# Performance work log

Hardware: AMD Instinct MI355X
Metric: run time of the kernel (lower is better)

Reference implementation:

```python
import jax, jax.numpy as jnp
import numpy as np

B, L, N_IN, N_STATE = 32, 4096, 8, 8
C_IN, C_OUT = N_IN + N_STATE, N_STATE
H, M, N_LAYERS = 64, 64, 4


def setup_inputs() -> dict:
    key = jax.random.key(0)
    ks = jax.random.split(key, 16)
    s = 0.02
    return {
        "u": jax.random.normal(ks[0], (B, L, N_IN), jnp.float32),
        "z": jax.random.normal(ks[1], (B, N_STATE), jnp.float32),
        "t": jax.random.uniform(ks[2], (B, 1), jnp.float32),
        "w_lift": jax.random.normal(ks[3], (H, C_IN), jnp.float32) * s,
        "b_lift": jnp.zeros((H,), jnp.float32),
        "spec_wr": jax.random.normal(ks[4], (N_LAYERS, H, H, M), jnp.float32) / (H),
        "spec_wi": jax.random.normal(ks[5], (N_LAYERS, H, H, M), jnp.float32) / (H),
        "w_skip": jax.random.normal(ks[6], (N_LAYERS, H, H), jnp.float32) * s,
        "b_skip": jnp.zeros((N_LAYERS, H), jnp.float32),
        "w_p1": jax.random.normal(ks[7], (2 * H, H), jnp.float32) * s,
        "b_p1": jnp.zeros((2 * H,), jnp.float32),
        "w_p2": jax.random.normal(ks[8], (C_OUT, 2 * H), jnp.float32) * s,
        "b_p2": jnp.zeros((C_OUT,), jnp.float32),
    }


def _fno_forward(u, z, w_lift, b_lift, spec_wr, spec_wi, w_skip, b_skip, w_p1, b_p1, w_p2, b_p2):
    b, l, _ = u.shape
    rep_z = jnp.broadcast_to(z[:, None, :], (b, l, z.shape[1]))
    x = jnp.concatenate([u, rep_z], axis=-1)          # [B, L, C_in]
    x = jnp.transpose(x, (0, 2, 1))                   # [B, C_in, L]
    # lifting (1x1 conv)
    x = jnp.einsum("bcl,hc->bhl", x, w_lift) + b_lift[None, :, None]
    n_layers, _, _, m = spec_wr.shape
    for i in range(n_layers):
        xf = jnp.fft.rfft(x, axis=-1)                 # [B, H, L//2+1] complex
        w = spec_wr[i] + 1j * spec_wi[i]              # [H, H, M]
        of = jnp.einsum("bim,oim->bom", xf[..., :m], w)
        of = jnp.pad(of, ((0, 0), (0, 0), (0, xf.shape[-1] - m)))
        xs = jnp.fft.irfft(of, n=l, axis=-1)          # [B, H, L]
        sk = jnp.einsum("bil,oi->bol", x, w_skip[i]) + b_skip[i][None, :, None]
        x = xs + sk
        if i < n_layers - 1:
            x = jax.nn.gelu(x)
    # projection: H -> 2H -> C_out (1x1 convs)
    x = jax.nn.gelu(jnp.einsum("bhl,ph->bpl", x, w_p1) + b_p1[None, :, None])
    x = jnp.einsum("bpl,op->bol", x, w_p2) + b_p2[None, :, None]
    outs = jnp.transpose(x, (0, 2, 1))                # [B, L, C_out]
    return outs[:, -1, :]                             # [B, C_out]


def reference(u, z, t, w_lift, b_lift, spec_wr, spec_wi, w_skip, b_skip, w_p1, b_p1, w_p2, b_p2):
    # t is accepted by the original forward but unused in FNOProjection
    return _fno_forward(u, z, w_lift, b_lift, spec_wr, spec_wi, w_skip, b_skip, w_p1, b_p1, w_p2, b_p2)
```

## Files before the change

### kernel.cpp

```cpp
#include <hip/hip_runtime.h>
#include <math.h>

typedef _Float16 f16;
typedef f16  f16x2 __attribute__((ext_vector_type(2)));
typedef f16  f16x4 __attribute__((ext_vector_type(4)));
typedef f16  f16x8 __attribute__((ext_vector_type(8)));
typedef float f32x4 __attribute__((ext_vector_type(4)));

#define F4(p)  (*(float4*)(p))
#define CF4(p) (*(const float4*)(p))

namespace {
constexpr int LL = 4096;
constexpr int HH = 64;

__device__ __forceinline__ float gelu_fast(float x) {
    float inner = 0.7978845608028654f * (x + 0.044715f * x * x * x);
    float e = __expf(-2.0f * inner);
    return x / (1.0f + e);
}

__device__ __forceinline__ f32x4 mfma16(f16x8 a, f16x8 b, f32x4 c) {
    return __builtin_amdgcn_mfma_f32_16x16x32_f16(a, b, c, 0, 0, 0);
}
}

__global__ __launch_bounds__(256) void k_init(const float* __restrict__ u,
                                              const float* __restrict__ z,
                                              const float* __restrict__ wl,
                                              const float* __restrict__ bl,
                                              const float* __restrict__ wsk,
                                              const float* __restrict__ wr,
                                              const float* __restrict__ wi,
                                              f16* __restrict__ Tdt,
                                              f16* __restrict__ Ttr,
                                              f16* __restrict__ wskh,
                                              f16* __restrict__ wrh,
                                              f16* __restrict__ wih,
                                              f16* __restrict__ XT0) {
    const int bid = blockIdx.x;
    const int t = threadIdx.x;
    if (bid < 512) {
        const int b = bid >> 4;
        const int l0 = (bid & 15) * 256;
        constexpr int IP = 260;
        __shared__ float in_s[16 * IP];
        __shared__ float wsh[64 * 16];
        __shared__ float bsh[64];
        for (int i = t; i < 1024; i += 256) wsh[i] = wl[i];
        if (t < 64) bsh[t] = bl[t];
#pragma unroll
        for (int q = 0; q < 2; ++q) {
            int f = t + q * 256;
            int l = f >> 1, cq = (f & 1) * 4;
            float4 v = CF4(u + ((size_t)b * LL + l0 + l) * 8 + cq);
            in_s[(cq + 0) * IP + l] = v.x;
            in_s[(cq + 1) * IP + l] = v.y;
            in_s[(cq + 2) * IP + l] = v.z;
            in_s[(cq + 3) * IP + l] = v.w;
        }
        for (int f = t; f < 8 * 256; f += 256) {
            int c = f >> 8, l = f & 255;
            in_s[(8 + c) * IP + l] = z[b * 8 + c];
        }
        __syncthreads();
        const int hg = t >> 5, lsub = t & 31;
        float acc[8][8] = {};
        for (int c = 0; c < 16; ++c) {
            float wv[8], inv[8];
#pragma unroll
            for (int i = 0; i < 8; ++i) wv[i] = wsh[(hg * 8 + i) * 16 + c];
#pragma unroll
            for (int j = 0; j < 8; ++j) inv[j] = in_s[c * IP + lsub + 32 * j];
#pragma unroll
            for (int i = 0; i < 8; ++i)
#pragma unroll
                for (int j = 0; j < 8; ++j) acc[i][j] += wv[i] * inv[j];
        }
#pragma unroll
        for (int j = 0; j < 8; ++j) {
            __attribute__((aligned(16))) f16 hv[8];
#pragma unroll
            for (int i = 0; i < 8; ++i) hv[i] = (f16)(acc[i][j] + bsh[hg * 8 + i]);
            int l = l0 + lsub + 32 * j;
            F4(XT0 + ((size_t)b * LL + l) * HH + hg * 8) = CF4(hv);
        }
    } else if (bid < 1536) {
        const int tb = bid - 512;
        const float w0 = 6.283185307179586f / 4096.0f;
        {
            int m = tb >> 4;
            int l = ((tb & 15) << 8) + t;
            float s, c;
            sincosf((float)((l * m) & 4095) * w0, &s, &c);
            Tdt[(size_t)(2 * m) * LL + l]     = (f16)c;
            Tdt[(size_t)(2 * m + 1) * LL + l] = (f16)(-s);
        }
        {
            int l = tb * 4 + (t >> 6);
            int m = t & 63;
            float s, c;
            sincosf((float)((l * m) & 4095) * w0, &s, &c);
            const float sc = 1.0f / 4096.0f;
            f16x2 pv;
            pv.x = (f16)((m == 0) ? sc : 2.0f * sc * c);
            pv.y = (f16)((m == 0) ? 0.0f : -2.0f * sc * s);
            *(f16x2*)(Ttr + (size_t)l * 128 + 2 * m) = pv;
        }
        if (tb < 64) {
            int idx = tb * 256 + t;
            wskh[idx] = (f16)wsk[idx];
        }
    } else {
        const int cb = bid - 1536;
        size_t base = (size_t)cb * 1024 + t * 4;
        float4 vr = CF4(wr + base);
        float4 vi = CF4(wi + base);
        f16x4 hr, hi;
        hr.x = (f16)vr.x; hr.y = (f16)vr.y; hr.z = (f16)vr.z; hr.w = (f16)vr.w;
        hi.x = (f16)vi.x; hi.y = (f16)vi.y; hi.z = (f16)vi.z; hi.w = (f16)vi.w;
        *(f16x4*)(wrh + base) = hr;
        *(f16x4*)(wih + base) = hi;
    }
}

__global__ __launch_bounds__(256) void k_dft(const f16* __restrict__ XT,
                                             const f16* __restrict__ Tdt,
                                             f16* __restrict__ Y) {
    __shared__ f16 Asl[32 * 72];
    __shared__ f16 Bsl[128 * 72];
    const int t = threadIdx.x;
    const int ch = blockIdx.x >> 1, h0 = (blockIdx.x & 1) * 32, b = blockIdx.y;
    const int lane = t & 63, wid = t >> 6;
    const int mh = (wid & 1) * 16, n0 = (wid >> 1) * 64;
    const int fm = lane & 15, fq = lane >> 4;
    f32x4 acc[4] = {};
    for (int k0 = 0; k0 < 512; k0 += 64) {
        const int l0 = ch * 512 + k0;
        __syncthreads();
        {
            int seg = t >> 6;
            f16x8 v = *(const f16x8*)(XT + ((size_t)b * LL + l0 + lane) * HH + h0 + seg * 8);
#pragma unroll
            for (int i = 0; i < 8; ++i) Asl[(seg * 8 + i) * 72 + lane] = v[i];
        }
#pragma unroll
        for (int p = 0; p < 4; ++p) {
            int r = (t >> 3) + p * 32;
            F4(&Bsl[r * 72 + (t & 7) * 8]) = CF4(Tdt + (size_t)r * LL + l0 + (t & 7) * 8);
        }
        __syncthreads();
#pragma unroll
        for (int ks = 0; ks < 64; ks += 32) {
            f16x8 a = *(const f16x8*)&Asl[(mh + fm) * 72 + ks + fq * 8];
#pragma unroll
            for (int j = 0; j < 4; ++j) {
                f16x8 bj = *(const f16x8*)&Bsl[(n0 + j * 16 + fm) * 72 + ks + fq * 8];
                acc[j] = mfma16(a, bj, acc[j]);
            }
        }
    }
    f16* yp = Y + ((size_t)ch * 2048 + b * HH + h0) * 128;
#pragma unroll
    for (int j = 0; j < 4; ++j)
#pragma unroll
        for (int r = 0; r < 4; ++r)
            yp[(size_t)(mh + fq * 4 + r) * 128 + n0 + j * 16 + fm] = (f16)acc[j][r];
}

__global__ __launch_bounds__(256) void k_spec(const f16* __restrict__ Y,
                                              const f16* __restrict__ wrh,
                                              const f16* __restrict__ wih,
                                              f16* __restrict__ Ofh, int layer) {
    __shared__ float xsh[64 * 128];
    const int t = threadIdx.x;
    const int b = blockIdx.x;
    const int og = blockIdx.y;
    {
#pragma unroll
        for (int i = 0; i < 4; ++i) {
            int g = t + i * 256;
            float s[8] = {};
#pragma unroll
            for (int c = 0; c < 8; ++c) {
                f16x8 v = *(const f16x8*)(Y + ((size_t)c * 2048 + b * HH) * 128 + g * 8);
#pragma unroll
                for (int e = 0; e < 8; ++e) s[e] += (float)v[e];
            }
#pragma unroll
            for (int e = 0; e < 8; ++e) xsh[g * 8 + e] = s[e];
        }
    }
    __syncthreads();
    const int m = t & 63, osub = t >> 6;
    const int o = og * 4 + osub;
    const f16* wrp = wrh + ((size_t)layer * HH + o) * HH * 64 + m;
    const f16* wip = wih + ((size_t)layer * HH + o) * HH * 64 + m;
    float are = 0.0f, aim = 0.0f;
    const float2* xs2 = (const float2*)xsh;
#pragma unroll 8
    for (int i = 0; i < 64; ++i) {
        float2 xv = xs2[i * 64 + m];
        float wrv = (float)wrp[(size_t)i * 64];
        float wiv = (float)wip[(size_t)i * 64];
        are += xv.x * wrv - xv.y * wiv;
        aim += xv.x * wiv + xv.y * wrv;
    }
    f16x2 ov; ov.x = (f16)are; ov.y = (f16)aim;
    *(f16x2*)(Ofh + ((size_t)b * HH + o) * 128 + 2 * m) = ov;
}

__global__ __launch_bounds__(256) void k_recon(const f16* __restrict__ Ofh,
                                               const f16* __restrict__ XT,
                                               const f16* __restrict__ Ttr,
                                               const f16* __restrict__ wskh,
                                               const float* __restrict__ bsk,
                                               f16* __restrict__ XTn,
                                               int layer) {
    __shared__ f16 Asl[64 * 200];
    __shared__ f16 Bsl[128 * 72];
    const int t = threadIdx.x;
    const int l0 = blockIdx.x * 128, b = blockIdx.y;
    const int lane = t & 63, wid = t >> 6;
    const int m0 = (wid & 1) * 32, n0 = (wid >> 1) * 64;
    const int fm = lane & 15, fq = lane >> 4;
    f32x4 acc[2][4] = {};
    {
        int seg = t & 15, row = t >> 4;
#pragma unroll
        for (int p = 0; p < 4; ++p) {
            int r = row + p * 16;
            F4(&Asl[r * 200 + seg * 8]) = CF4(Ofh + ((size_t)(b * HH + r)) * 128 + seg * 8);
        }
        int seg8 = t & 7, row8 = t >> 3;
#pragma unroll
        for (int p = 0; p < 2; ++p) {
            int r = row8 + p * 32;
            F4(&Asl[r * 200 + 128 + seg8 * 8]) =
                CF4(wskh + ((size_t)(layer * HH + r)) * HH + seg8 * 8);
        }
    }
    const int srow = t >> 3, sseg = t & 7;
    for (int k0 = 0; k0 < 192; k0 += 64) {
        __syncthreads();
#pragma unroll
        for (int p = 0; p < 4; ++p) {
            int r = srow + p * 32;
            const f16* src = (k0 < 128)
                ? (Ttr + (size_t)(l0 + r) * 128 + k0 + sseg * 8)
                : (XT + ((size_t)b * LL + l0 + r) * HH + sseg * 8);
            F4(&Bsl[r * 72 + sseg * 8]) = CF4(src);
        }
        __syncthreads();
#pragma unroll
        for (int ks = 0; ks < 64; ks += 32) {
            f16x8 a0 = *(const f16x8*)&Asl[(m0 + fm) * 200 + k0 + ks + fq * 8];
            f16x8 a1 = *(const f16x8*)&Asl[(m0 + 16 + fm) * 200 + k0 + ks + fq * 8];
#pragma unroll
            for (int j = 0; j < 4; ++j) {
                f16x8 bj = *(const f16x8*)&Bsl[(n0 + j * 16 + fm) * 72 + ks + fq * 8];
                acc[0][j] = mfma16(a0, bj, acc[0][j]);
                acc[1][j] = mfma16(a1, bj, acc[1][j]);
            }
        }
    }
    __syncthreads();
#pragma unroll
    for (int i = 0; i < 2; ++i)
#pragma unroll
        for (int r = 0; r < 4; ++r) {
            int row = m0 + i * 16 + fq * 4 + r;
            float bias = bsk[layer * HH + row];
#pragma unroll
            for (int j = 0; j < 4; ++j) {
                float v = gelu_fast(acc[i][j][r] + bias);
                int lc = n0 + j * 16 + fm;
                Bsl[lc * 72 + row] = (f16)v;
            }
        }
    __syncthreads();
    {
        int row = t >> 1, half = t & 1;
        f16* dst = XTn + ((size_t)b * LL + l0 + row) * HH + half * 32;
        const f16* src = &Bsl[row * 72 + half * 32];
#pragma unroll
        for (int i = 0; i < 4; ++i)
            F4(dst + i * 8) = CF4(src + i * 8);
    }
}

__global__ __launch_bounds__(128) void k_final(const f16* __restrict__ Ofh,
                                               const f16* __restrict__ XT3,
                                               const f16* __restrict__ Ttr,
                                               const float* __restrict__ wsk,
                                               const float* __restrict__ bsk,
                                               const float* __restrict__ wp1,
                                               const float* __restrict__ bp1,
                                               const float* __restrict__ wp2,
                                               const float* __restrict__ bp2,
                                               float* __restrict__ out) {
    __shared__ float ofs[64 * 129];
    __shared__ float wsks[64 * 65];
    __shared__ float wp1s[128 * 65];
    __shared__ float tl[128], xl[64], x4[64], y[128];
    const int b = blockIdx.x, t = threadIdx.x;
    {
#pragma unroll
        for (int i = 0; i < 8; ++i) {
            int g = t + i * 128;
            f16x8 v = *(const f16x8*)(Ofh + (size_t)b * HH * 128 + g * 8);
            int o = g >> 4, k0 = (g & 15) * 8;
#pragma unroll
            for (int e = 0; e < 8; ++e) ofs[o * 129 + k0 + e] = (float)v[e];
        }
    }
    {
        const float* src = wsk + 3 * HH * HH;
#pragma unroll
        for (int i = 0; i < 8; ++i) {
            int g = t + i * 128;
            float4 v = CF4(src + g * 4);
            int o = g >> 4, c0 = (g & 15) * 4;
            F4(&wsks[o * 65 + c0]) = v;
        }
    }
    {
#pragma unroll
        for (int i = 0; i < 16; ++i) {
            int g = t + i * 128;
            float4 v = CF4(wp1 + g * 4);
            int p = g >> 4, c0 = (g & 15) * 4;
            F4(&wp1s[p * 65 + c0]) = v;
        }
    }
    tl[t] = (float)Ttr[(size_t)(LL - 1) * 128 + t];
    if (t < 64) xl[t] = (float)XT3[((size_t)b * LL + (LL - 1)) * HH + t];
    __syncthreads();
    if (t < 64) {
        const int o = t;
        float acc = bsk[3 * HH + o];
        for (int k = 0; k < 128; ++k) acc += ofs[o * 129 + k] * tl[k];
        for (int i = 0; i < 64; ++i) acc += wsks[o * 65 + i] * xl[i];
        x4[o] = acc;
    }
    __syncthreads();
    {
        float acc = bp1[t];
        for (int h = 0; h < 64; ++h) acc += wp1s[t * 65 + h] * x4[h];
        y[t] = gelu_fast(acc);
    }
    __syncthreads();
    if (t < 8) {
        float acc = bp2[t];
        for (int p = 0; p < 128; ++p) acc += wp2[t * 128 + p] * y[p];
        out[b * 8 + t] = acc;
    }
}

extern "C" void kernel_launch(void* const* d_in, const int* in_sizes, int n_in,
                              void* d_out, int out_size, void* d_ws, size_t ws_size,
                              hipStream_t stream) {
    (void)in_sizes; (void)n_in; (void)out_size; (void)ws_size;
    const float* u   = (const float*)d_in[0];
    const float* z   = (const float*)d_in[1];
    const float* wl  = (const float*)d_in[3];
    const float* bl  = (const float*)d_in[4];
    const float* swr = (const float*)d_in[5];
    const float* swi = (const float*)d_in[6];
    const float* wsk = (const float*)d_in[7];
    const float* bsk = (const float*)d_in[8];
    const float* wp1 = (const float*)d_in[9];
    const float* bp1 = (const float*)d_in[10];
    const float* wp2 = (const float*)d_in[11];
    const float* bp2 = (const float*)d_in[12];
    float* out = (float*)d_out;

    f16* ws    = (f16*)d_ws;
    f16* XTa   = ws;
    f16* XTb   = XTa + 8388608;
    f16* Tdt   = XTb + 8388608;
    f16* Ttr   = Tdt + 524288;
    f16* Ofh   = Ttr + 524288;
    f16* wskh  = Ofh + 262144;
    f16* wrh   = wskh + 16384;
    f16* wih   = wrh + 1048576;

    k_init<<<2560, 256, 0, stream>>>(u, z, wl, bl, wsk, swr, swi,
                                     Tdt, Ttr, wskh, wrh, wih, XTa);

    f16* xtc = XTa; f16* xtn = XTb;
    for (int layer = 0; layer < 4; ++layer) {
        f16* Y = xtn;
        k_dft<<<dim3(16, 32), 256, 0, stream>>>(xtc, Tdt, Y);
        k_spec<<<dim3(32, 16), 256, 0, stream>>>(Y, wrh, wih, Ofh, layer);
        if (layer < 3) {
            k_recon<<<dim3(32, 32), 256, 0, stream>>>(Ofh, xtc, Ttr, wskh, bsk,
                                                      xtn, layer);
            f16* tmp = xtc; xtc = xtn; xtn = tmp;
        } else {
            k_final<<<32, 128, 0, stream>>>(Ofh, xtc, Ttr, wsk, bsk,
                                            wp1, bp1, wp2, bp2, out);
        }
    }
}
```

Measured before the change: 213.4 us.

## Fuse truncated forward DFT into lifting and reconstruction kernels

New measurement: 248.5 us. 16.5% more time.

```diff
diff --git a/kernel.cpp b/kernel.cpp
--- a/kernel.cpp
+++ b/kernel.cpp
@@ -25,68 +25,18 @@
 }
 }
 
-__global__ __launch_bounds__(256) void k_init(const float* __restrict__ u,
-                                              const float* __restrict__ z,
-                                              const float* __restrict__ wl,
-                                              const float* __restrict__ bl,
-                                              const float* __restrict__ wsk,
-                                              const float* __restrict__ wr,
-                                              const float* __restrict__ wi,
-                                              f16* __restrict__ Tdt,
-                                              f16* __restrict__ Ttr,
-                                              f16* __restrict__ wskh,
-                                              f16* __restrict__ wrh,
-                                              f16* __restrict__ wih,
-                                              f16* __restrict__ XT0) {
+__global__ __launch_bounds__(256) void k_tw(const float* __restrict__ wsk,
+                                            const float* __restrict__ wr,
+                                            const float* __restrict__ wi,
+                                            f16* __restrict__ Tdt,
+                                            f16* __restrict__ Ttr,
+                                            f16* __restrict__ wskh,
+                                            f16* __restrict__ wrh,
+                                            f16* __restrict__ wih) {
     const int bid = blockIdx.x;
     const int t = threadIdx.x;
-    if (bid < 512) {
-        const int b = bid >> 4;
-        const int l0 = (bid & 15) * 256;
-        constexpr int IP = 260;
-        __shared__ float in_s[16 * IP];
-        __shared__ float wsh[64 * 16];
-        __shared__ float bsh[64];
-        for (int i = t; i < 1024; i += 256) wsh[i] = wl[i];
-        if (t < 64) bsh[t] = bl[t];
-#pragma unroll
-        for (int q = 0; q < 2; ++q) {
-            int f = t + q * 256;
-            int l = f >> 1, cq = (f & 1) * 4;
-            float4 v = CF4(u + ((size_t)b * LL + l0 + l) * 8 + cq);
-            in_s[(cq + 0) * IP + l] = v.x;
-            in_s[(cq + 1) * IP + l] = v.y;
-            in_s[(cq + 2) * IP + l] = v.z;
-            in_s[(cq + 3) * IP + l] = v.w;
-        }
-        for (int f = t; f < 8 * 256; f += 256) {
-            int c = f >> 8, l = f & 255;
-            in_s[(8 + c) * IP + l] = z[b * 8 + c];
-        }
-        __syncthreads();
-        const int hg = t >> 5, lsub = t & 31;
-        float acc[8][8] = {};
-        for (int c = 0; c < 16; ++c) {
-            float wv[8], inv[8];
-#pragma unroll
-            for (int i = 0; i < 8; ++i) wv[i] = wsh[(hg * 8 + i) * 16 + c];
-#pragma unroll
-            for (int j = 0; j < 8; ++j) inv[j] = in_s[c * IP + lsub + 32 * j];
-#pragma unroll
-            for (int i = 0; i < 8; ++i)
-#pragma unroll
-                for (int j = 0; j < 8; ++j) acc[i][j] += wv[i] * inv[j];
-        }
-#pragma unroll
-        for (int j = 0; j < 8; ++j) {
-            __attribute__((aligned(16))) f16 hv[8];
-#pragma unroll
-            for (int i = 0; i < 8; ++i) hv[i] = (f16)(acc[i][j] + bsh[hg * 8 + i]);
-            int l = l0 + lsub + 32 * j;
-            F4(XT0 + ((size_t)b * LL + l) * HH + hg * 8) = CF4(hv);
-        }
-    } else if (bid < 1536) {
-        const int tb = bid - 512;
+    if (bid < 1024) {
+        const int tb = bid;
         const float w0 = 6.283185307179586f / 4096.0f;
         {
             int m = tb >> 4;
@@ -112,7 +62,7 @@
             wskh[idx] = (f16)wsk[idx];
         }
     } else {
-        const int cb = bid - 1536;
+        const int cb = bid - 1024;
         size_t base = (size_t)cb * 1024 + t * 4;
         float4 vr = CF4(wr + base);
         float4 vi = CF4(wi + base);
@@ -124,48 +74,102 @@
     }
 }
 
-__global__ __launch_bounds__(256) void k_dft(const f16* __restrict__ XT,
-                                             const f16* __restrict__ Tdt,
-                                             f16* __restrict__ Y) {
-    __shared__ f16 Asl[32 * 72];
-    __shared__ f16 Bsl[128 * 72];
+__global__ __launch_bounds__(256) void k_lift(const float* __restrict__ u,
+                                              const float* __restrict__ z,
+                                              const float* __restrict__ wl,
+                                              const float* __restrict__ bl,
+                                              const f16* __restrict__ Tdt,
+                                              f16* __restrict__ XT0,
+                                              f16* __restrict__ Y) {
+    __shared__ __attribute__((aligned(16))) f16 pool[26112];
+    __shared__ float bsh[64];
+    float* in_s = (float*)pool;
+    float* wsh  = (float*)pool + 4160;
+    f16* Xh  = pool;
+    f16* Bsl = pool + 16896;
+    constexpr int IP = 260;
     const int t = threadIdx.x;
-    const int ch = blockIdx.x >> 1, h0 = (blockIdx.x & 1) * 32, b = blockIdx.y;
+    const int lt = blockIdx.x, b = blockIdx.y;
+    const int l0 = lt * 256;
+    for (int i = t; i < 1024; i += 256) wsh[i] = wl[i];
+    if (t < 64) bsh[t] = bl[t];
+#pragma unroll
+    for (int q = 0; q < 2; ++q) {
+        int f = t + q * 256;
+        int l = f >> 1, cq = (f & 1) * 4;
+        float4 v = CF4(u + ((size_t)b * LL + l0 + l) * 8 + cq);
+        in_s[(cq + 0) * IP + l] = v.x;
+        in_s[(cq + 1) * IP + l] = v.y;
+        in_s[(cq + 2) * IP + l] = v.z;
+        in_s[(cq + 3) * IP + l] = v.w;
+    }
+    for (int f = t; f < 8 * 256; f += 256) {
+        int c = f >> 8, l = f & 255;
+        in_s[(8 + c) * IP + l] = z[b * 8 + c];
+    }
+    __syncthreads();
+    const int hg = t >> 5, lsub = t & 31;
+    float acc[8][8] = {};
+    for (int c = 0; c < 16; ++c) {
+        float wv[8], inv[8];
+#pragma unroll
+        for (int i = 0; i < 8; ++i) wv[i] = wsh[(hg * 8 + i) * 16 + c];
+#pragma unroll
+        for (int j = 0; j < 8; ++j) inv[j] = in_s[c * IP + lsub + 32 * j];
+#pragma unroll
+        for (int i = 0; i < 8; ++i)
+#pragma unroll
+            for (int j = 0; j < 8; ++j) acc[i][j] += wv[i] * inv[j];
+    }
+    __syncthreads();
+#pragma unroll
+    for (int j = 0; j < 8; ++j) {
+        __attribute__((aligned(16))) f16 hv[8];
+#pragma unroll
+        for (int i = 0; i < 8; ++i) hv[i] = (f16)(acc[i][j] + bsh[hg * 8 + i]);
+        int l = l0 + lsub + 32 * j;
+        F4(XT0 + ((size_t)b * LL + l) * HH + hg * 8) = CF4(hv);
+#pragma unroll
+        for (int i = 0; i < 8; ++i)
+            Xh[(hg * 8 + i) * 264 + lsub + 32 * j] = hv[i];
+    }
     const int lane = t & 63, wid = t >> 6;
-    const int mh = (wid & 1) * 16, n0 = (wid >> 1) * 64;
     const int fm = lane & 15, fq = lane >> 4;
-    f32x4 acc[4] = {};
-    for (int k0 = 0; k0 < 512; k0 += 64) {
-        const int l0 = ch * 512 + k0;
-        __syncthreads();
-        {
-            int seg = t >> 6;
-            f16x8 v = *(const f16x8*)(XT + ((size_t)b * LL + l0 + lane) * HH + h0 + seg * 8);
-#pragma unroll
-            for (int i = 0; i < 8; ++i) Asl[(seg * 8 + i) * 72 + lane] = v[i];
-        }
-#pragma unroll
-        for (int p = 0; p < 4; ++p) {
-            int r = (t >> 3) + p * 32;
-            F4(&Bsl[r * 72 + (t & 7) * 8]) = CF4(Tdt + (size_t)r * LL + l0 + (t & 7) * 8);
-        }
-        __syncthreads();
-#pragma unroll
-        for (int ks = 0; ks < 64; ks += 32) {
-            f16x8 a = *(const f16x8*)&Asl[(mh + fm) * 72 + ks + fq * 8];
-#pragma unroll
-            for (int j = 0; j < 4; ++j) {
-                f16x8 bj = *(const f16x8*)&Bsl[(n0 + j * 16 + fm) * 72 + ks + fq * 8];
-                acc[j] = mfma16(a, bj, acc[j]);
-            }
-        }
-    }
-    f16* yp = Y + ((size_t)ch * 2048 + b * HH + h0) * 128;
-#pragma unroll
-    for (int j = 0; j < 4; ++j)
-#pragma unroll
-        for (int r = 0; r < 4; ++r)
-            yp[(size_t)(mh + fq * 4 + r) * 128 + n0 + j * 16 + fm] = (f16)acc[j][r];
+    const int n0d = wid * 32;
+    for (int half = 0; half < 2; ++half) {
+        f32x4 acc2[4][2] = {};
+        for (int kc = 0; kc < 2; ++kc) {
+            __syncthreads();
+#pragma unroll
+            for (int p = 0; p < 4; ++p) {
+                int r = (t >> 3) + p * 32;
+                F4(&Bsl[r * 72 + (t & 7) * 8]) =
+                    CF4(Tdt + (size_t)r * LL + l0 + half * 128 + kc * 64 + (t & 7) * 8);
+            }
+            __syncthreads();
+#pragma unroll
+            for (int ks = 0; ks < 64; ks += 32) {
+                f16x8 a[4];
+#pragma unroll
+                for (int i = 0; i < 4; ++i)
+                    a[i] = *(const f16x8*)&Xh[(fm + 16 * i) * 264 + half * 128 + kc * 64 + ks + fq * 8];
+#pragma unroll
+                for (int j = 0; j < 2; ++j) {
+                    f16x8 bj = *(const f16x8*)&Bsl[(n0d + j * 16 + fm) * 72 + ks + fq * 8];
+#pragma unroll
+                    for (int i = 0; i < 4; ++i) acc2[i][j] = mfma16(a[i], bj, acc2[i][j]);
+                }
+            }
+        }
+        f16* yp = Y + ((size_t)(lt * 2 + half) * 2048 + b * 64) * 128;
+#pragma unroll
+        for (int i = 0; i < 4; ++i)
+#pragma unroll
+            for (int j = 0; j < 2; ++j)
+#pragma unroll
+                for (int r = 0; r < 4; ++r)
+                    yp[(size_t)(i * 16 + fq * 4 + r) * 128 + n0d + j * 16 + fm] = (f16)acc2[i][j][r];
+    }
 }
 
 __global__ __launch_bounds__(256) void k_spec(const f16* __restrict__ Y,
@@ -181,8 +185,7 @@
         for (int i = 0; i < 4; ++i) {
             int g = t + i * 256;
             float s[8] = {};
-#pragma unroll
-            for (int c = 0; c < 8; ++c) {
+            for (int c = 0; c < 32; ++c) {
                 f16x8 v = *(const f16x8*)(Y + ((size_t)c * 2048 + b * HH) * 128 + g * 8);
 #pragma unroll
                 for (int e = 0; e < 8; ++e) s[e] += (float)v[e];
@@ -213,14 +216,20 @@
 __global__ __launch_bounds__(256) void k_recon(const f16* __restrict__ Ofh,
                                                const f16* __restrict__ XT,
                                                const f16* __restrict__ Ttr,
+                                               const f16* __restrict__ Tdt,
                                                const f16* __restrict__ wskh,
                                                const float* __restrict__ bsk,
                                                f16* __restrict__ XTn,
+                                               f16* __restrict__ Y,
                                                int layer) {
-    __shared__ f16 Asl[64 * 200];
-    __shared__ f16 Bsl[128 * 72];
+    __shared__ __attribute__((aligned(16))) f16 pool[27136];
+    f16* Amain = pool;
+    f16* Bmain = pool + 12800;
+    f16* Ash   = pool;
+    f16* Xsl   = pool + 8704;
+    f16* B2    = pool + 17920;
     const int t = threadIdx.x;
-    const int l0 = blockIdx.x * 128, b = blockIdx.y;
+    const int lt = blockIdx.x, l0 = lt * 128, b = blockIdx.y;
     const int lane = t & 63, wid = t >> 6;
     const int m0 = (wid & 1) * 32, n0 = (wid >> 1) * 64;
     const int fm = lane & 15, fq = lane >> 4;
@@ -230,13 +239,13 @@
 #pragma unroll
         for (int p = 0; p < 4; ++p) {
             int r = row + p * 16;
-            F4(&Asl[r * 200 + seg * 8]) = CF4(Ofh + ((size_t)(b * HH + r)) * 128 + seg * 8);
+            F4(&Amain[r * 200 + seg * 8]) = CF4(Ofh + ((size_t)(b * HH + r)) * 128 + seg * 8);
         }
         int seg8 = t & 7, row8 = t >> 3;
 #pragma unroll
         for (int p = 0; p < 2; ++p) {
             int r = row8 + p * 32;
-            F4(&Asl[r * 200 + 128 + seg8 * 8]) =
+            F4(&Amain[r * 200 + 128 + seg8 * 8]) =
                 CF4(wskh + ((size_t)(layer * HH + r)) * HH + seg8 * 8);
         }
     }
@@ -249,16 +258,16 @@
             const f16* src = (k0 < 128)
                 ? (Ttr + (size_t)(l0 + r) * 128 + k0 + sseg * 8)
                 : (XT + ((size_t)b * LL + l0 + r) * HH + sseg * 8);
-            F4(&Bsl[r * 72 + sseg * 8]) = CF4(src);
+            F4(&Bmain[r * 72 + sseg * 8]) = CF4(src);
         }
         __syncthreads();
 #pragma unroll
         for (int ks = 0; ks < 64; ks += 32) {
-            f16x8 a0 = *(const f16x8*)&Asl[(m0 + fm) * 200 + k0 + ks + fq * 8];
-            f16x8 a1 = *(const f16x8*)&Asl[(m0 + 16 + fm) * 200 + k0 + ks + fq * 8];
+            f16x8 a0 = *(const f16x8*)&Amain[(m0 + fm) * 200 + k0 + ks + fq * 8];
+            f16x8 a1 = *(const f16x8*)&Amain[(m0 + 16 + fm) * 200 + k0 + ks + fq * 8];
 #pragma unroll
             for (int j = 0; j < 4; ++j) {
-                f16x8 bj = *(const f16x8*)&Bsl[(n0 + j * 16 + fm) * 72 + ks + fq * 8];
+                f16x8 bj = *(const f16x8*)&Bmain[(n0 + j * 16 + fm) * 72 + ks + fq * 8];
                 acc[0][j] = mfma16(a0, bj, acc[0][j]);
                 acc[1][j] = mfma16(a1, bj, acc[1][j]);
             }
@@ -274,19 +283,54 @@
 #pragma unroll
             for (int j = 0; j < 4; ++j) {
                 float v = gelu_fast(acc[i][j][r] + bias);
+                f16 hv = (f16)v;
                 int lc = n0 + j * 16 + fm;
-                Bsl[lc * 72 + row] = (f16)v;
+                Xsl[lc * 72 + row] = hv;
+                Ash[row * 136 + lc] = hv;
             }
         }
     __syncthreads();
     {
         int row = t >> 1, half = t & 1;
         f16* dst = XTn + ((size_t)b * LL + l0 + row) * HH + half * 32;
-        const f16* src = &Bsl[row * 72 + half * 32];
+        const f16* src = &Xsl[row * 72 + half * 32];
 #pragma unroll
         for (int i = 0; i < 4; ++i)
             F4(dst + i * 8) = CF4(src + i * 8);
     }
+    const int n0d = wid * 32;
+    f32x4 acc2[4][2] = {};
+    for (int kc = 0; kc < 2; ++kc) {
+        __syncthreads();
+#pragma unroll
+        for (int p = 0; p < 4; ++p) {
+            int r = (t >> 3) + p * 32;
+            F4(&B2[r * 72 + (t & 7) * 8]) =
+                CF4(Tdt + (size_t)r * LL + l0 + kc * 64 + (t & 7) * 8);
+        }
+        __syncthreads();
+#pragma unroll
+        for (int ks = 0; ks < 64; ks += 32) {
+            f16x8 a[4];
+#pragma unroll
+            for (int i = 0; i < 4; ++i)
+                a[i] = *(const f16x8*)&Ash[(fm + 16 * i) * 136 + kc * 64 + ks + fq * 8];
+#pragma unroll
+            for (int j = 0; j < 2; ++j) {
+                f16x8 bj = *(const f16x8*)&B2[(n0d + j * 16 + fm) * 72 + ks + fq * 8];
+#pragma unroll
+                for (int i = 0; i < 4; ++i) acc2[i][j] = mfma16(a[i], bj, acc2[i][j]);
+            }
+        }
+    }
+    f16* yp = Y + ((size_t)lt * 2048 + b * 64) * 128;
+#pragma unroll
+    for (int i = 0; i < 4; ++i)
+#pragma unroll
+        for (int j = 0; j < 2; ++j)
+#pragma unroll
+            for (int r = 0; r < 4; ++r)
+                yp[(size_t)(i * 16 + fq * 4 + r) * 128 + n0d + j * 16 + fm] = (f16)acc2[i][j][r];
 }
 
 __global__ __launch_bounds__(128) void k_final(const f16* __restrict__ Ofh,
@@ -378,24 +422,23 @@
     f16* ws    = (f16*)d_ws;
     f16* XTa   = ws;
     f16* XTb   = XTa + 8388608;
-    f16* Tdt   = XTb + 8388608;
+    f16* Yb    = XTb + 8388608;
+    f16* Tdt   = Yb + 8388608;
     f16* Ttr   = Tdt + 524288;
     f16* Ofh   = Ttr + 524288;
     f16* wskh  = Ofh + 262144;
     f16* wrh   = wskh + 16384;
     f16* wih   = wrh + 1048576;
 
-    k_init<<<2560, 256, 0, stream>>>(u, z, wl, bl, wsk, swr, swi,
-                                     Tdt, Ttr, wskh, wrh, wih, XTa);
+    k_tw<<<2048, 256, 0, stream>>>(wsk, swr, swi, Tdt, Ttr, wskh, wrh, wih);
+    k_lift<<<dim3(16, 32), 256, 0, stream>>>(u, z, wl, bl, Tdt, XTa, Yb);
 
     f16* xtc = XTa; f16* xtn = XTb;
     for (int layer = 0; layer < 4; ++layer) {
-        f16* Y = xtn;
-        k_dft<<<dim3(16, 32), 256, 0, stream>>>(xtc, Tdt, Y);
-        k_spec<<<dim3(32, 16), 256, 0, stream>>>(Y, wrh, wih, Ofh, layer);
+        k_spec<<<dim3(32, 16), 256, 0, stream>>>(Yb, wrh, wih, Ofh, layer);
         if (layer < 3) {
-            k_recon<<<dim3(32, 32), 256, 0, stream>>>(Ofh, xtc, Ttr, wskh, bsk,
-                                                      xtn, layer);
+            k_recon<<<dim3(32, 32), 256, 0, stream>>>(Ofh, xtc, Ttr, Tdt, wskh,
+                                                      bsk, xtn, Yb, layer);
             f16* tmp = xtc; xtc = xtn; xtn = tmp;
         } else {
             k_final<<<32, 128, 0, stream>>>(Ofh, xtc, Ttr, wsk, bsk,
```

## Fuse DFT and spectral mixing into a single kernel without split-L partials

Applied to the files above, without the earlier changes.

After: 317.0 us. 48.6% more time.

```diff
diff --git a/kernel.cpp b/kernel.cpp
--- a/kernel.cpp
+++ b/kernel.cpp
@@ -124,90 +124,69 @@
     }
 }
 
-__global__ __launch_bounds__(256) void k_dft(const f16* __restrict__ XT,
-                                             const f16* __restrict__ Tdt,
-                                             f16* __restrict__ Y) {
-    __shared__ f16 Asl[32 * 72];
-    __shared__ f16 Bsl[128 * 72];
+__global__ __launch_bounds__(1024) void k_dftspec(const f16* __restrict__ XT,
+                                                  const f16* __restrict__ Tdt,
+                                                  const f16* __restrict__ wrh,
+                                                  const f16* __restrict__ wih,
+                                                  f16* __restrict__ Ofh, int layer) {
+    __shared__ __attribute__((aligned(16))) f16 pool[17408];
+    f16* Asl = pool;
+    f16* Bsl = pool + 8704;
+    float* xsh = (float*)pool;
+    const int bid = blockIdx.x;
+    const int b = bid & 31, mhalf = bid >> 5;
     const int t = threadIdx.x;
-    const int ch = blockIdx.x >> 1, h0 = (blockIdx.x & 1) * 32, b = blockIdx.y;
-    const int lane = t & 63, wid = t >> 6;
-    const int mh = (wid & 1) * 16, n0 = (wid >> 1) * 64;
+    const int wid = t >> 6, lane = t & 63;
+    const int wm = wid & 3, wn = wid >> 2;
     const int fm = lane & 15, fq = lane >> 4;
-    f32x4 acc[4] = {};
-    for (int k0 = 0; k0 < 512; k0 += 64) {
-        const int l0 = ch * 512 + k0;
-        __syncthreads();
-        {
-            int seg = t >> 6;
-            f16x8 v = *(const f16x8*)(XT + ((size_t)b * LL + l0 + lane) * HH + h0 + seg * 8);
-#pragma unroll
-            for (int i = 0; i < 8; ++i) Asl[(seg * 8 + i) * 72 + lane] = v[i];
-        }
-#pragma unroll
-        for (int p = 0; p < 4; ++p) {
-            int r = (t >> 3) + p * 32;
-            F4(&Bsl[r * 72 + (t & 7) * 8]) = CF4(Tdt + (size_t)r * LL + l0 + (t & 7) * 8);
-        }
-        __syncthreads();
-#pragma unroll
-        for (int ks = 0; ks < 64; ks += 32) {
-            f16x8 a = *(const f16x8*)&Asl[(mh + fm) * 72 + ks + fq * 8];
-#pragma unroll
-            for (int j = 0; j < 4; ++j) {
-                f16x8 bj = *(const f16x8*)&Bsl[(n0 + j * 16 + fm) * 72 + ks + fq * 8];
-                acc[j] = mfma16(a, bj, acc[j]);
-            }
-        }
-    }
-    f16* yp = Y + ((size_t)ch * 2048 + b * HH + h0) * 128;
-#pragma unroll
-    for (int j = 0; j < 4; ++j)
-#pragma unroll
-        for (int r = 0; r < 4; ++r)
-            yp[(size_t)(mh + fq * 4 + r) * 128 + n0 + j * 16 + fm] = (f16)acc[j][r];
-}
-
-__global__ __launch_bounds__(256) void k_spec(const f16* __restrict__ Y,
-                                              const f16* __restrict__ wrh,
-                                              const f16* __restrict__ wih,
-                                              f16* __restrict__ Ofh, int layer) {
-    __shared__ float xsh[64 * 128];
-    const int t = threadIdx.x;
-    const int b = blockIdx.x;
-    const int og = blockIdx.y;
-    {
-#pragma unroll
-        for (int i = 0; i < 4; ++i) {
-            int g = t + i * 256;
-            float s[8] = {};
-#pragma unroll
-            for (int c = 0; c < 8; ++c) {
-                f16x8 v = *(const f16x8*)(Y + ((size_t)c * 2048 + b * HH) * 128 + g * 8);
-#pragma unroll
-                for (int e = 0; e < 8; ++e) s[e] += (float)v[e];
-            }
-#pragma unroll
-            for (int e = 0; e < 8; ++e) xsh[g * 8 + e] = s[e];
-        }
-    }
-    __syncthreads();
-    const int m = t & 63, osub = t >> 6;
-    const int o = og * 4 + osub;
-    const f16* wrp = wrh + ((size_t)layer * HH + o) * HH * 64 + m;
-    const f16* wip = wih + ((size_t)layer * HH + o) * HH * 64 + m;
-    float are = 0.0f, aim = 0.0f;
-    const float2* xs2 = (const float2*)xsh;
+    const int sa_seg = t >> 7, sa_l = t & 127;
+    const int sb_row = t >> 4, sb_seg = t & 15;
+
+    f16x8 ra = *(const f16x8*)(XT + ((size_t)b * LL + sa_l) * HH + sa_seg * 8);
+    f16x8 rb = *(const f16x8*)(Tdt + (size_t)(mhalf * 64 + sb_row) * LL + sb_seg * 8);
+    f32x4 acc = {};
+    for (int c = 0; c < 32; ++c) {
+        __syncthreads();
+#pragma unroll
+        for (int i = 0; i < 8; ++i) Asl[(sa_seg * 8 + i) * 136 + sa_l] = ra[i];
+        *(f16x8*)&Bsl[sb_row * 136 + sb_seg * 8] = rb;
+        __syncthreads();
+        if (c < 31) {
+            int l0 = (c + 1) * 128;
+            ra = *(const f16x8*)(XT + ((size_t)b * LL + l0 + sa_l) * HH + sa_seg * 8);
+            rb = *(const f16x8*)(Tdt + (size_t)(mhalf * 64 + sb_row) * LL + l0 + sb_seg * 8);
+        }
+#pragma unroll
+        for (int ks = 0; ks < 128; ks += 32) {
+            f16x8 a  = *(const f16x8*)&Asl[(wm * 16 + fm) * 136 + ks + fq * 8];
+            f16x8 bv = *(const f16x8*)&Bsl[(wn * 16 + fm) * 136 + ks + fq * 8];
+            acc = mfma16(a, bv, acc);
+        }
+    }
+    __syncthreads();
+#pragma unroll
+    for (int r = 0; r < 4; ++r)
+        xsh[(wm * 16 + fq * 4 + r) * 66 + wn * 16 + fm] = acc[r];
+    __syncthreads();
+    const int mloc = t & 31, og = t >> 5;
+    const int mg = mhalf * 32 + mloc;
+    const f16* wr0 = wrh + ((size_t)(layer * HH + og) * HH) * 64 + mg;
+    const f16* wi0 = wih + ((size_t)(layer * HH + og) * HH) * 64 + mg;
+    const f16* wr1 = wr0 + (size_t)32 * HH * 64;
+    const f16* wi1 = wi0 + (size_t)32 * HH * 64;
+    float are0 = 0, aim0 = 0, are1 = 0, aim1 = 0;
 #pragma unroll 8
     for (int i = 0; i < 64; ++i) {
-        float2 xv = xs2[i * 64 + m];
-        float wrv = (float)wrp[(size_t)i * 64];
-        float wiv = (float)wip[(size_t)i * 64];
-        are += xv.x * wrv - xv.y * wiv;
-        aim += xv.x * wiv + xv.y * wrv;
-    }
-    f16x2 ov; ov.x = (f16)are; ov.y = (f16)aim;
-    *(f16x2*)(Ofh + ((size_t)b * HH + o) * 128 + 2 * m) = ov;
+        float2 xv = *(const float2*)&xsh[i * 66 + 2 * mloc];
+        float w0r = (float)wr0[(size_t)i * 64], w0i = (float)wi0[(size_t)i * 64];
+        float w1r = (float)wr1[(size_t)i * 64], w1i = (float)wi1[(size_t)i * 64];
+        are0 += xv.x * w0r - xv.y * w0i;  aim0 += xv.x * w0i + xv.y * w0r;
+        are1 += xv.x * w1r - xv.y * w1i;  aim1 += xv.x * w1i + xv.y * w1r;
+    }
+    f16x2 o0; o0.x = (f16)are0; o0.y = (f16)aim0;
+    f16x2 o1; o1.x = (f16)are1; o1.y = (f16)aim1;
+    *(f16x2*)(Ofh + ((size_t)b * HH + og) * 128 + 2 * mg)      = o0;
+    *(f16x2*)(Ofh + ((size_t)b * HH + og + 32) * 128 + 2 * mg) = o1;
 }
 
 __global__ __launch_bounds__(256) void k_recon(const f16* __restrict__ Ofh,
@@ -390,9 +369,7 @@
 
     f16* xtc = XTa; f16* xtn = XTb;
     for (int layer = 0; layer < 4; ++layer) {
-        f16* Y = xtn;
-        k_dft<<<dim3(16, 32), 256, 0, stream>>>(xtc, Tdt, Y);
-        k_spec<<<dim3(32, 16), 256, 0, stream>>>(Y, wrh, wih, Ofh, layer);
+        k_dftspec<<<64, 1024, 0, stream>>>(xtc, Tdt, wrh, wih, Ofh, layer);
         if (layer < 3) {
             k_recon<<<dim3(32, 32), 256, 0, stream>>>(Ofh, xtc, Ttr, wskh, bsk,
                                                       xtn, layer);
```
